# Kernel tuning notes

Measured on AMD Instinct MI355X. Metric: run time of the kernel, lower is better.

The kernel has to match this reference:

```python
import jax, jax.numpy as jnp
import numpy as np

# --- solver / dynamics constants (from HopfieldLayer source) ---
DT0 = 0.1          # constructor dt
TOL = 0.01         # RKF56Solver tol
MIN_DT = 0.1       # RKF56Solver min_dt
MAX_DELTA_T = 50.0 # stop_condition max delta t
VEL_TOL = 0.05     # stop_condition relaxation tolerance
MAX_STEPS = 32     # fixed step budget for jit-compatible scan

# Runge-Kutta-Fehlberg embedded pair coefficients (autonomous system)
A21 = 0.25
A31, A32 = 3.0/32.0, 9.0/32.0
A41, A42, A43 = 1932.0/2197.0, -7200.0/2197.0, 7296.0/2197.0
A51, A52, A53, A54 = 439.0/216.0, -8.0, 3680.0/513.0, -845.0/4104.0
A61, A62, A63, A64, A65 = -8.0/27.0, 2.0, -3544.0/2565.0, 1859.0/4104.0, -11.0/40.0
# high-order solution weights
B1, B3, B4, B5, B6 = 16.0/135.0, 6656.0/12825.0, 28561.0/56430.0, -9.0/50.0, 2.0/55.0
# low-order solution weights (for error estimate)
C1, C3, C4, C5 = 25.0/216.0, 1408.0/2565.0, 2197.0/4104.0, -1.0/5.0


def setup_inputs() -> dict:
    key = jax.random.key(0)
    k1, k2 = jax.random.split(key)
    B, D = 512, 512
    x0 = jax.random.normal(k1, (B, D), dtype=jnp.float32)
    # dense fn weights, scaled ~1/sqrt(D) like a trained layer
    W = jax.random.normal(k2, (D, D), dtype=jnp.float32) * (1.0 / np.sqrt(D))
    b = jnp.zeros((D,), dtype=jnp.float32)
    return {"x0": x0, "W": W, "b": b}


def reference(x0, W, b):
    d = x0.shape[-1]

    def pvf(x):
        # -grad_x mean(x^2 + tanh(xW + b), axis=-1), analytic form
        z = x @ W + b                      # [B, D]
        sech2 = 1.0 - jnp.tanh(z) ** 2
        return -(2.0 * x + sech2 @ W.T) / d

    def rkf_step(x, dt):
        k1 = pvf(x)
        k2 = pvf(x + dt * (A21 * k1))
        k3 = pvf(x + dt * (A31 * k1 + A32 * k2))
        k4 = pvf(x + dt * (A41 * k1 + A42 * k2 + A43 * k3))
        k5 = pvf(x + dt * (A51 * k1 + A52 * k2 + A53 * k3 + A54 * k4))
        k6 = pvf(x + dt * (A61 * k1 + A62 * k2 + A63 * k3 + A64 * k4 + A65 * k5))
        x_hi = x + dt * (B1 * k1 + B3 * k3 + B4 * k4 + B5 * k5 + B6 * k6)
        x_lo = x + dt * (C1 * k1 + C3 * k3 + C4 * k4 + C5 * k5)
        err = jnp.max(jnp.abs(x_hi - x_lo))
        return x_hi, err

    def body(carry, _):
        t, x, dt, done = carry
        x_new, err = rkf_step(x, dt)
        accept = (err < TOL) | (dt <= MIN_DT)
        t2 = jnp.where(accept, t + dt, t)
        x2 = jnp.where(accept, x_new, x)
        # adaptive step-size update, clipped at min_dt and growth factor 2
        factor = jnp.clip(0.9 * (TOL / (err + 1e-12)) ** 0.2, 0.2, 2.0)
        dt_next = jnp.maximum(dt * factor, MIN_DT)
        # stop conditions from the original module
        max_abs_vel = jnp.mean(jnp.max(jnp.abs(pvf(x2)), axis=-1))
        done_new = done | (t2 > MAX_DELTA_T) | (max_abs_vel < VEL_TOL)
        # freeze state once done
        t_out = jnp.where(done, t, t2)
        x_out = jnp.where(done, x, x2)
        dt_out = jnp.where(done, dt, dt_next)
        return (t_out, x_out, dt_out, done_new), None

    init = (jnp.float32(0.0), x0, jnp.float32(DT0), jnp.array(False))
    (t, x, dt, done), _ = jax.lax.scan(body, init, None, length=MAX_STEPS)
    return x
```

## Files before the change

kernel.cpp:

```cpp
#include <hip/hip_runtime.h>
#include <hip/hip_cooperative_groups.h>
#include <hip/hip_fp16.h>
#include <math.h>

namespace cg = cooperative_groups;

#define DIM   512
#define NBLK  128
#define NTHR  1024
#define NROW  4
#define KP    256
#define KHALF 128

typedef _Float16 h2 __attribute__((ext_vector_type(2)));

#if __has_builtin(__builtin_amdgcn_fdot2)
__device__ __forceinline__ float dot2f(unsigned a, unsigned b, float c){
  return __builtin_amdgcn_fdot2(__builtin_bit_cast(h2, a), __builtin_bit_cast(h2, b), c, false);
}
#else
__device__ __forceinline__ float dot2f(unsigned au, unsigned bu, float c){
  h2 a = __builtin_bit_cast(h2, au), b = __builtin_bit_cast(h2, bu);
  return fmaf((float)a[0], (float)b[0], fmaf((float)a[1], (float)b[1], c));
}
#endif

constexpr float cA21 = 0.25f;
constexpr float cA31 = (float)(3.0/32.0),     cA32 = (float)(9.0/32.0);
constexpr float cA41 = (float)(1932.0/2197.0),cA42 = (float)(-7200.0/2197.0), cA43 = (float)(7296.0/2197.0);
constexpr float cA51 = (float)(439.0/216.0),  cA52 = -8.0f,                   cA53 = (float)(3680.0/513.0), cA54 = (float)(-845.0/4104.0);
constexpr float cA61 = (float)(-8.0/27.0),    cA62 = 2.0f,                    cA63 = (float)(-3544.0/2565.0), cA64 = (float)(1859.0/4104.0), cA65 = (float)(-11.0/40.0);
constexpr float cB1 = (float)(16.0/135.0), cB3 = (float)(6656.0/12825.0), cB4 = (float)(28561.0/56430.0), cB5 = (float)(-9.0/50.0), cB6 = (float)(2.0/55.0);
constexpr float cC1 = (float)(25.0/216.0), cC3 = (float)(1408.0/2565.0),  cC4 = (float)(2197.0/4104.0),  cC5 = -0.2f;

constexpr float TOLf = 0.01f, MIN_DTf = 0.1f, DT0f = 0.1f, MAXTf = 50.0f, VELTOLf = 0.05f;
constexpr float INVD = 1.0f/512.0f;

__device__ __forceinline__ unsigned packh(float a, float b){
  unsigned short lo = __half_as_ushort(__float2half(a));
  unsigned short hi = __half_as_ushort(__float2half(b));
  return (unsigned)lo | ((unsigned)hi << 16);
}

__device__ __forceinline__ void gbar(unsigned* ctr, int tid){
  __syncthreads();
  if (tid == 0){
    __hip_atomic_fetch_add(ctr, 1u, __ATOMIC_RELEASE, __HIP_MEMORY_SCOPE_AGENT);
    unsigned v;
    do {
      __builtin_amdgcn_s_sleep(2);
      v = __hip_atomic_load(ctr, __ATOMIC_RELAXED, __HIP_MEMORY_SCOPE_AGENT);
    } while (v < NBLK);
    (void)__hip_atomic_load(ctr, __ATOMIC_ACQUIRE, __HIP_MEMORY_SCOPE_AGENT);
  }
  __syncthreads();
}

__global__ void __launch_bounds__(NTHR, 1)
hop_kernel(const float* __restrict__ x0, const float* __restrict__ W,
           const float* __restrict__ bvec, float* __restrict__ out,
           unsigned char* __restrict__ ws)
{
  cg::grid_group grid = cg::this_grid();

  unsigned*           bar  = (unsigned*)ws;
  unsigned*           errs = (unsigned*)(ws + 384);
  unsigned long long* vels = (unsigned long long*)(ws + 512);
  unsigned*           Wq   = (unsigned*)(ws + 4096);
  unsigned*           WTq  = Wq + KP*DIM;

  const int tid  = threadIdx.x;
  const int b    = blockIdx.x;
  const int wid  = tid >> 6;
  const int lane = tid & 63;

  const int mc = tid & 511;
  const int mh = tid >> 9;
  const int pr   = tid >> 8;
  const int pc   = tid & 255;
  const int colA = pc << 1;
  const int grow = b*NROW + pr;

  __shared__ __align__(16) unsigned pkY[KP*NROW];
  __shared__ __align__(16) unsigned pkS[KP*NROW];
  __shared__ float sPart[2*NROW*DIM];
  __shared__ float red[32];
  __shared__ float bcast[4];

  {
    int e  = b*NTHR + tid;
    int kp = e >> 9, c = e & 511;
    size_t qi = (size_t)(kp >> 2)*2048 + (size_t)c*4 + (kp & 3);
    Wq[qi] = packh(W[(size_t)(2*kp)*DIM + c], W[(size_t)(2*kp+1)*DIM + c]);
    float2 wt = *reinterpret_cast<const float2*>(W + (size_t)c*DIM + 2*kp);
    WTq[qi] = packh(wt.x, wt.y);
  }

  float x[2], bv[2];
  { float2 xx = *reinterpret_cast<const float2*>(x0 + (size_t)grow*DIM + colA);
    x[0]=xx.x; x[1]=xx.y; }
  { float2 b2 = *reinterpret_cast<const float2*>(bvec + colA);
    bv[0]=b2.x; bv[1]=b2.y; }

  grid.sync();

  float t = 0.f, dt = DT0f;
  float k1[2],k2[2],k3[2],k4[2],k5[2],xhi[2],yreg[2];

  auto mm_store = [&](const unsigned* __restrict__ Wp, const unsigned (&pk)[KP*NROW]){
    float a0=0.f, a1=0.f, a2=0.f, a3=0.f;
    const int kbase = mh * KHALF;
    const unsigned* wp = Wp + (size_t)(kbase >> 2)*2048 + (size_t)mc*4;
    #pragma unroll 4
    for (int kt = 0; kt < KHALF/4; ++kt){
      const int kp0 = kbase + kt*4;
      uint4 w  = *reinterpret_cast<const uint4*>(wp); wp += 2048;
      uint4 y0 = *reinterpret_cast<const uint4*>(&pk[(kp0+0)*NROW]);
      uint4 y1 = *reinterpret_cast<const uint4*>(&pk[(kp0+1)*NROW]);
      uint4 y2 = *reinterpret_cast<const uint4*>(&pk[(kp0+2)*NROW]);
      uint4 y3 = *reinterpret_cast<const uint4*>(&pk[(kp0+3)*NROW]);
      a0 = dot2f(w.x, y0.x, a0); a1 = dot2f(w.x, y0.y, a1); a2 = dot2f(w.x, y0.z, a2); a3 = dot2f(w.x, y0.w, a3);
      a0 = dot2f(w.y, y1.x, a0); a1 = dot2f(w.y, y1.y, a1); a2 = dot2f(w.y, y1.z, a2); a3 = dot2f(w.y, y1.w, a3);
      a0 = dot2f(w.z, y2.x, a0); a1 = dot2f(w.z, y2.y, a1); a2 = dot2f(w.z, y2.z, a2); a3 = dot2f(w.z, y2.w, a3);
      a0 = dot2f(w.w, y3.x, a0); a1 = dot2f(w.w, y3.y, a1); a2 = dot2f(w.w, y3.z, a2); a3 = dot2f(w.w, y3.w, a3);
    }
    sPart[(mh*NROW + 0)*DIM + mc] = a0;
    sPart[(mh*NROW + 1)*DIM + mc] = a1;
    sPart[(mh*NROW + 2)*DIM + mc] = a2;
    sPart[(mh*NROW + 3)*DIM + mc] = a3;
  };

  auto comb = [&](float g[2]){
    float2 p0 = *reinterpret_cast<const float2*>(&sPart[(0*NROW + pr)*DIM + colA]);
    float2 p1 = *reinterpret_cast<const float2*>(&sPart[(1*NROW + pr)*DIM + colA]);
    g[0] = p0.x + p1.x; g[1] = p0.y + p1.y;
  };

  auto set_y = [&](float y0, float y1){
    yreg[0] = y0; yreg[1] = y1;
    pkY[pc*NROW + pr] = packh(y0, y1);
    __syncthreads();
  };
  auto run_fwd = [&](){
    mm_store(Wq, pkY);
    __syncthreads();
    float g[2]; comb(g);
    float th0 = tanhf(g[0] + bv[0]);
    float th1 = tanhf(g[1] + bv[1]);
    pkS[pc*NROW + pr] = packh(1.f - th0*th0, 1.f - th1*th1);
    __syncthreads();
  };
  auto run_bwd = [&](float ko[2]){
    mm_store(WTq, pkS);
    __syncthreads();
    float g[2]; comb(g);
    ko[0] = -(2.f*yreg[0] + g[0]) * INVD;
    ko[1] = -(2.f*yreg[1] + g[1]) * INVD;
  };

  for (int iter = 0; iter < 32; ++iter){
    set_y(x[0], x[1]);
    run_fwd(); run_bwd(k1);
    set_y(x[0]+dt*(cA21*k1[0]), x[1]+dt*(cA21*k1[1]));
    run_fwd(); run_bwd(k2);
    set_y(x[0]+dt*(cA31*k1[0]+cA32*k2[0]), x[1]+dt*(cA31*k1[1]+cA32*k2[1]));
    run_fwd(); run_bwd(k3);
    set_y(x[0]+dt*(cA41*k1[0]+cA42*k2[0]+cA43*k3[0]),
          x[1]+dt*(cA41*k1[1]+cA42*k2[1]+cA43*k3[1]));
    run_fwd(); run_bwd(k4);
    set_y(x[0]+dt*(cA51*k1[0]+cA52*k2[0]+cA53*k3[0]+cA54*k4[0]),
          x[1]+dt*(cA51*k1[1]+cA52*k2[1]+cA53*k3[1]+cA54*k4[1]));
    run_fwd(); run_bwd(k5);

    set_y(x[0]+dt*(cA61*k1[0]+cA62*k2[0]+cA63*k3[0]+cA64*k4[0]+cA65*k5[0]),
          x[1]+dt*(cA61*k1[1]+cA62*k2[1]+cA63*k3[1]+cA64*k4[1]+cA65*k5[1]));
    run_fwd();
    mm_store(WTq, pkS);
    __syncthreads();
    {
      float g[2]; comb(g);
      float emax = 0.f;
      #pragma unroll
      for (int i = 0; i < 2; ++i){
        float k6 = -(2.f*yreg[i] + g[i]) * INVD;
        float hi = x[i] + dt*(cB1*k1[i] + cB3*k3[i] + cB4*k4[i] + cB5*k5[i] + cB6*k6);
        float lo = x[i] + dt*(cC1*k1[i] + cC3*k3[i] + cC4*k4[i] + cC5*k5[i]);
        xhi[i] = hi;
        emax = fmaxf(emax, fabsf(hi - lo));
      }
      #pragma unroll
      for (int s = 32; s > 0; s >>= 1) emax = fmaxf(emax, __shfl_xor(emax, s, 64));
      if (lane == 0) red[wid] = emax;
      __syncthreads();
      if (tid == 0){
        float m = red[0];
        #pragma unroll
        for (int wv = 1; wv < 16; ++wv) m = fmaxf(m, red[wv]);
        atomicMax(&errs[iter], __float_as_uint(m));
      }
    }

    gbar(&bar[2*iter], tid);
    if (tid == 0)
      bcast[0] = __uint_as_float(__hip_atomic_load(&errs[iter], __ATOMIC_RELAXED, __HIP_MEMORY_SCOPE_AGENT));
    __syncthreads();
    const float err = bcast[0];
    const bool accept = (err < TOLf) || (dt <= MIN_DTf);
    if (accept){ x[0]=xhi[0]; x[1]=xhi[1]; }

    set_y(x[0], x[1]);
    run_fwd();
    mm_store(WTq, pkS);
    __syncthreads();
    {
      float g[2]; comb(g);
      float vmax = fmaxf(fabsf(-(2.f*x[0] + g[0]) * INVD),
                         fabsf(-(2.f*x[1] + g[1]) * INVD));
      #pragma unroll
      for (int s = 32; s > 0; s >>= 1) vmax = fmaxf(vmax, __shfl_xor(vmax, s, 64));
      if (lane == 0) red[wid] = vmax;
      __syncthreads();
      if (tid == 0){
        double rsum = 0.0;
        #pragma unroll
        for (int rr = 0; rr < NROW; ++rr){
          float rm = fmaxf(fmaxf(red[4*rr], red[4*rr+1]), fmaxf(red[4*rr+2], red[4*rr+3]));
          rsum += (double)rm;
        }
        unsigned long long fx = (unsigned long long)(rsum * 4294967296.0);
        atomicAdd(&vels[iter], fx);
      }
    }

    gbar(&bar[2*iter+1], tid);
    if (tid == 0){
      unsigned long long sv = __hip_atomic_load(&vels[iter], __ATOMIC_RELAXED, __HIP_MEMORY_SCOPE_AGENT);
      float vel = (float)((double)sv * (1.0/4294967296.0) / 512.0);
      float t2  = accept ? (t + dt) : t;
      float factor = 0.9f * powf(TOLf / (err + 1e-12f), 0.2f);
      factor = fminf(fmaxf(factor, 0.2f), 2.0f);
      float dtn = fmaxf(dt * factor, MIN_DTf);
      bcast[0] = t2; bcast[1] = dtn;
      bcast[2] = ((t2 > MAXTf) || (vel < VELTOLf)) ? 1.f : 0.f;
    }
    __syncthreads();
    t = bcast[0]; dt = bcast[1];
    if (bcast[2] != 0.f) break;
  }

  float2 o; o.x = x[0]; o.y = x[1];
  *reinterpret_cast<float2*>(out + (size_t)grow*DIM + colA) = o;
}

extern "C" void kernel_launch(void* const* d_in, const int* in_sizes, int n_in,
                              void* d_out, int out_size, void* d_ws, size_t ws_size,
                              hipStream_t stream)
{
  const float* x0 = (const float*)d_in[0];
  const float* W  = (const float*)d_in[1];
  const float* bv = (const float*)d_in[2];
  float* out = (float*)d_out;
  unsigned char* ws = (unsigned char*)d_ws;

  hipMemsetAsync(ws, 0, 4096, stream);

  void* args[] = { (void*)&x0, (void*)&W, (void*)&bv, (void*)&out, (void*)&ws };
  (void)in_sizes; (void)n_in; (void)out_size; (void)ws_size;
  hipLaunchCooperativeKernel((void*)hop_kernel, dim3(NBLK), dim3(NTHR), args, 0, stream);
}
```

Measured before the change: 144.9 us.

## Retile matvec into 4x4 register blocks with 8-way K split and reuse velocity as k1

Each thread now computes a 4-row by 4-column block over one of eight K slices instead of one column over half of K. Each global weight load is therefore reused across four rows, which cuts per-FMA load traffic, at the cost of a larger partial-sum buffer and an 8-way combine. The packed activation layout changes to row-major so each row slice is a contiguous vector load. The velocity evaluation at the end of each step now also produces k1 for the next step, removing one forward/backward pass per iteration. That reuse matches the reference only when the step is not frozen by the done flag.

New measurement: 236.7 us. +63.3%, slower.

```diff
diff --git a/kernel.cpp b/kernel.cpp
--- a/kernel.cpp
+++ b/kernel.cpp
@@ -10,7 +10,8 @@
 #define NTHR  1024
 #define NROW  4
 #define KP    256
-#define KHALF 128
+#define NKS   8
+#define KPT   32
 
 typedef _Float16 h2 __attribute__((ext_vector_type(2)));
 
@@ -56,6 +57,12 @@
   __syncthreads();
 }
 
+#define RC(r,c,wv,yv) \
+  acc[r][c] = dot2f(wv.x, yv.x, acc[r][c]); \
+  acc[r][c] = dot2f(wv.y, yv.y, acc[r][c]); \
+  acc[r][c] = dot2f(wv.z, yv.z, acc[r][c]); \
+  acc[r][c] = dot2f(wv.w, yv.w, acc[r][c]);
+
 __global__ void __launch_bounds__(NTHR, 1)
 hop_kernel(const float* __restrict__ x0, const float* __restrict__ W,
            const float* __restrict__ bvec, float* __restrict__ out,
@@ -74,16 +81,16 @@
   const int wid  = tid >> 6;
   const int lane = tid & 63;
 
-  const int mc = tid & 511;
-  const int mh = tid >> 9;
+  const int ks = tid >> 7;
+  const int cg = tid & 127;
   const int pr   = tid >> 8;
   const int pc   = tid & 255;
   const int colA = pc << 1;
   const int grow = b*NROW + pr;
 
-  __shared__ __align__(16) unsigned pkY[KP*NROW];
-  __shared__ __align__(16) unsigned pkS[KP*NROW];
-  __shared__ float sPart[2*NROW*DIM];
+  __shared__ __align__(16) unsigned pkY[NROW*KP];
+  __shared__ __align__(16) unsigned pkS[NROW*KP];
+  __shared__ __align__(16) float sPart[NKS*NROW*DIM];
   __shared__ float red[32];
   __shared__ float bcast[4];
 
@@ -107,38 +114,51 @@
   float t = 0.f, dt = DT0f;
   float k1[2],k2[2],k3[2],k4[2],k5[2],xhi[2],yreg[2];
 
-  auto mm_store = [&](const unsigned* __restrict__ Wp, const unsigned (&pk)[KP*NROW]){
-    float a0=0.f, a1=0.f, a2=0.f, a3=0.f;
-    const int kbase = mh * KHALF;
-    const unsigned* wp = Wp + (size_t)(kbase >> 2)*2048 + (size_t)mc*4;
-    #pragma unroll 4
-    for (int kt = 0; kt < KHALF/4; ++kt){
-      const int kp0 = kbase + kt*4;
-      uint4 w  = *reinterpret_cast<const uint4*>(wp); wp += 2048;
-      uint4 y0 = *reinterpret_cast<const uint4*>(&pk[(kp0+0)*NROW]);
-      uint4 y1 = *reinterpret_cast<const uint4*>(&pk[(kp0+1)*NROW]);
-      uint4 y2 = *reinterpret_cast<const uint4*>(&pk[(kp0+2)*NROW]);
-      uint4 y3 = *reinterpret_cast<const uint4*>(&pk[(kp0+3)*NROW]);
-      a0 = dot2f(w.x, y0.x, a0); a1 = dot2f(w.x, y0.y, a1); a2 = dot2f(w.x, y0.z, a2); a3 = dot2f(w.x, y0.w, a3);
-      a0 = dot2f(w.y, y1.x, a0); a1 = dot2f(w.y, y1.y, a1); a2 = dot2f(w.y, y1.z, a2); a3 = dot2f(w.y, y1.w, a3);
-      a0 = dot2f(w.z, y2.x, a0); a1 = dot2f(w.z, y2.y, a1); a2 = dot2f(w.z, y2.z, a2); a3 = dot2f(w.z, y2.w, a3);
-      a0 = dot2f(w.w, y3.x, a0); a1 = dot2f(w.w, y3.y, a1); a2 = dot2f(w.w, y3.z, a2); a3 = dot2f(w.w, y3.w, a3);
-    }
-    sPart[(mh*NROW + 0)*DIM + mc] = a0;
-    sPart[(mh*NROW + 1)*DIM + mc] = a1;
-    sPart[(mh*NROW + 2)*DIM + mc] = a2;
-    sPart[(mh*NROW + 3)*DIM + mc] = a3;
+  auto mm_store = [&](const unsigned* __restrict__ Wp, const unsigned* __restrict__ pk){
+    float acc[4][4];
+    #pragma unroll
+    for (int r = 0; r < 4; ++r)
+      #pragma unroll
+      for (int c = 0; c < 4; ++c) acc[r][c] = 0.f;
+    const unsigned* wp = Wp + (size_t)(ks*8)*2048 + (size_t)cg*16;
+    const int kb = ks*KPT;
+    #pragma unroll
+    for (int ch = 0; ch < 8; ++ch){
+      const int kpc = kb + ch*4;
+      uint4 w0 = *reinterpret_cast<const uint4*>(wp + 0);
+      uint4 w1 = *reinterpret_cast<const uint4*>(wp + 4);
+      uint4 w2 = *reinterpret_cast<const uint4*>(wp + 8);
+      uint4 w3 = *reinterpret_cast<const uint4*>(wp + 12);
+      wp += 2048;
+      uint4 y0 = *reinterpret_cast<const uint4*>(&pk[0*KP + kpc]);
+      uint4 y1 = *reinterpret_cast<const uint4*>(&pk[1*KP + kpc]);
+      uint4 y2 = *reinterpret_cast<const uint4*>(&pk[2*KP + kpc]);
+      uint4 y3 = *reinterpret_cast<const uint4*>(&pk[3*KP + kpc]);
+      RC(0,0,w0,y0) RC(0,1,w1,y0) RC(0,2,w2,y0) RC(0,3,w3,y0)
+      RC(1,0,w0,y1) RC(1,1,w1,y1) RC(1,2,w2,y1) RC(1,3,w3,y1)
+      RC(2,0,w0,y2) RC(2,1,w1,y2) RC(2,2,w2,y2) RC(2,3,w3,y2)
+      RC(3,0,w0,y3) RC(3,1,w1,y3) RC(3,2,w2,y3) RC(3,3,w3,y3)
+    }
+    #pragma unroll
+    for (int r = 0; r < 4; ++r){
+      float4 v; v.x=acc[r][0]; v.y=acc[r][1]; v.z=acc[r][2]; v.w=acc[r][3];
+      *reinterpret_cast<float4*>(&sPart[(ks*NROW + r)*DIM + cg*4]) = v;
+    }
   };
 
   auto comb = [&](float g[2]){
-    float2 p0 = *reinterpret_cast<const float2*>(&sPart[(0*NROW + pr)*DIM + colA]);
-    float2 p1 = *reinterpret_cast<const float2*>(&sPart[(1*NROW + pr)*DIM + colA]);
-    g[0] = p0.x + p1.x; g[1] = p0.y + p1.y;
+    float s0 = 0.f, s1 = 0.f;
+    #pragma unroll
+    for (int kk = 0; kk < NKS; ++kk){
+      float2 p = *reinterpret_cast<const float2*>(&sPart[(kk*NROW + pr)*DIM + colA]);
+      s0 += p.x; s1 += p.y;
+    }
+    g[0] = s0; g[1] = s1;
   };
 
   auto set_y = [&](float y0, float y1){
     yreg[0] = y0; yreg[1] = y1;
-    pkY[pc*NROW + pr] = packh(y0, y1);
+    pkY[pr*KP + pc] = packh(y0, y1);
     __syncthreads();
   };
   auto run_fwd = [&](){
@@ -147,7 +167,7 @@
     float g[2]; comb(g);
     float th0 = tanhf(g[0] + bv[0]);
     float th1 = tanhf(g[1] + bv[1]);
-    pkS[pc*NROW + pr] = packh(1.f - th0*th0, 1.f - th1*th1);
+    pkS[pr*KP + pc] = packh(1.f - th0*th0, 1.f - th1*th1);
     __syncthreads();
   };
   auto run_bwd = [&](float ko[2]){
@@ -158,9 +178,10 @@
     ko[1] = -(2.f*yreg[1] + g[1]) * INVD;
   };
 
+  set_y(x[0], x[1]);
+  run_fwd(); run_bwd(k1);
+
   for (int iter = 0; iter < 32; ++iter){
-    set_y(x[0], x[1]);
-    run_fwd(); run_bwd(k1);
     set_y(x[0]+dt*(cA21*k1[0]), x[1]+dt*(cA21*k1[1]));
     run_fwd(); run_bwd(k2);
     set_y(x[0]+dt*(cA31*k1[0]+cA32*k2[0]), x[1]+dt*(cA31*k1[1]+cA32*k2[1]));
@@ -209,13 +230,9 @@
     if (accept){ x[0]=xhi[0]; x[1]=xhi[1]; }
 
     set_y(x[0], x[1]);
-    run_fwd();
-    mm_store(WTq, pkS);
-    __syncthreads();
+    run_fwd(); run_bwd(k1);
     {
-      float g[2]; comb(g);
-      float vmax = fmaxf(fabsf(-(2.f*x[0] + g[0]) * INVD),
-                         fabsf(-(2.f*x[1] + g[1]) * INVD));
+      float vmax = fmaxf(fabsf(k1[0]), fabsf(k1[1]));
       #pragma unroll
       for (int s = 32; s > 0; s >>= 1) vmax = fmaxf(vmax, __shfl_xor(vmax, s, 64));
       if (lane == 0) red[wid] = vmax;
```
